# Kernel optimization log

Measured on AMD Instinct MI355X. Metric: run time of the kernel, lower is better.

## Reference

```python
import math
import jax, jax.numpy as jnp
import numpy as np

NUM_HEADS = 12
ALPHA, BETA, GAMMA = 1.9, 3.8, 15.2  # get_rpe_config(ratio=1.9)
SKIP = 1


def _rp_bucket(side):
    """iRPE euclidean contextual bucket table for a side x side grid + 1 cls token."""
    beta_int = int(BETA)
    coords = np.stack(np.meshgrid(np.arange(side), np.arange(side), indexing='ij'), -1).reshape(-1, 2)
    diff = coords[:, None, :] - coords[None, :, :]
    dis = np.round(np.sqrt((diff ** 2).sum(-1).astype(np.float64)))  # rounded euclidean distance
    far = np.clip(np.round(ALPHA + np.log(np.maximum(dis, 1e-9) / ALPHA) / math.log(GAMMA / ALPHA) * (BETA - ALPHA)), None, BETA)
    idx = np.where(dis <= ALPHA, dis, far).astype(np.int32) + beta_int
    num_buckets = 2 * beta_int + 1  # 7
    L = side * side
    full = np.full((L + SKIP, L + SKIP), num_buckets, dtype=np.int32)  # extra bucket for cls
    full[SKIP:, SKIP:] = idx
    return full, num_buckets + 1  # table [P,P], total buckets = 8


def setup_inputs() -> dict:
    key = jax.random.key(0)
    ks = jax.random.split(key, 8)
    B, P, n_mod, C = 64, 197, 2, 768
    N = 1 + (P - 1) * n_mod  # 393
    hd = C // NUM_HEADS
    rp_bucket, n_buckets = _rp_bucket(int(math.sqrt(P - SKIP)))
    s = 0.02
    return {
        'x': jax.random.normal(ks[0], (B, N, C), jnp.float32),
        'q_learned': jax.random.normal(ks[1], (1, 1, C), jnp.float32) * s,
        'pos_embed': jax.random.normal(ks[2], (1, P, C), jnp.float32) * s,
        'wk': jax.random.normal(ks[3], (C, C), jnp.float32) * s,
        'wv': jax.random.normal(ks[4], (C, C), jnp.float32) * s,
        'rpe_w': jax.random.normal(ks[5], (hd, n_buckets), jnp.float32) * s,  # shared_head ctx lookup table
        'proj_w': jax.random.normal(ks[6], (C, C), jnp.float32) * s,
        'proj_b': jnp.zeros((C,), jnp.float32),
        'rp_bucket': jnp.asarray(rp_bucket),  # [P, P] int32
    }


def reference(x, q_learned, pos_embed, wk, wv, rpe_w, proj_w, proj_b, rp_bucket):
    B, N, C = x.shape
    H = NUM_HEADS
    hd = C // H
    P = rp_bucket.shape[0]
    n_mod = (N - 1) // (P - 1)
    scale = hd ** -0.5

    q_ = jnp.broadcast_to(q_learned + pos_embed, (B, P, C))
    q = q_.reshape(B, P, H, hd).transpose(0, 2, 1, 3)                    # bhpd
    k = (x @ wk.T).reshape(B, N, H, hd).transpose(0, 2, 1, 3)            # bhnd
    v = (x @ wv.T).reshape(B, N, H, hd).transpose(0, 2, 1, 3)            # bhnd

    attn = jnp.einsum('bhpd,bhnd->bhpn', q, k) * scale                   # [B,H,P,N]

    # contextual RPE on keys: lookup = q @ table, gathered by rp_bucket[i, j]
    lookup = jnp.einsum('bhpd,du->bhpu', q, rpe_w)                        # [B,H,P,n_buckets]
    bias = lookup[:, :, jnp.arange(P)[:, None], rp_bucket]                # [B,H,P,P]
    bias = jnp.concatenate([bias[..., :1], jnp.tile(bias[..., 1:], (1, 1, 1, n_mod))], axis=-1)
    attn = jax.nn.softmax(attn + bias, axis=-1)

    out = jnp.einsum('bhpn,bhnd->bhpd', attn, v).transpose(0, 2, 1, 3).reshape(B, P, C)
    return out @ proj_w.T + proj_b
```

## Files before the change

### kernel.cpp

```cpp
#include <hip/hip_runtime.h>

typedef unsigned short u16;
typedef short bf16x8 __attribute__((ext_vector_type(8)));
typedef float f32x4 __attribute__((ext_vector_type(4)));
typedef const __attribute__((address_space(1))) void* gptr_t;
typedef __attribute__((address_space(3))) void* lptr_t;

#define B_   64
#define N_   393
#define C_   768
#define H_   12
#define HD_  64
#define P_   197
#define BIAS_N 416
#define PPAD 208
#define VTP  448
#define M_KV (B_ * N_)
#define M_PR (B_ * P_)
#define SCALE_L2E 0.180336879f
#define PPITCH 70

__device__ __forceinline__ u16 f2bf(float f) {
    unsigned u = __float_as_uint(f);
    return (u16)((u + 0x7FFFu + ((u >> 16) & 1u)) >> 16);
}
__device__ __forceinline__ unsigned cvt_pk_bf16(float lo, float hi) {
    unsigned r;
    asm("v_cvt_pk_bf16_f32 %0, %1, %2" : "=v"(r) : "v"(lo), "v"(hi));
    return r;
}
__device__ __forceinline__ float exp2_fast(float x) {
    float r;
    asm("v_exp_f32 %0, %1" : "=v"(r) : "v"(x));
    return r;
}

__global__ __launch_bounds__(256) void conv_prep1(
    const float* __restrict__ x, const float* __restrict__ wk,
    const float* __restrict__ wv, const float* __restrict__ pw,
    const float* __restrict__ q_learned, const float* __restrict__ pos_embed,
    const float* __restrict__ rpe_w,
    u16* __restrict__ xh, u16* __restrict__ wkvh, u16* __restrict__ pwh,
    u16* __restrict__ qh, float* __restrict__ lk)
{
    __shared__ float q_s[C_];
    const int bx = blockIdx.x, t = threadIdx.x;
    if (bx < 20592) {
        const int XN4 = 19316736 / 4;
        const int WN4 = 589824 / 4;
        int i = bx * 256 + t;
        const float* src; u16* dst; int off;
        if (i < XN4) { src = x; dst = xh; off = i; }
        else {
            int j = i - XN4;
            int sec = j / WN4;
            off = j - sec * WN4;
            src = sec == 0 ? wk : (sec == 1 ? wv : pw);
            dst = sec == 0 ? wkvh : (sec == 1 ? wkvh + 589824 : pwh);
        }
        float4 v = ((const float4*)src)[off];
        u16 o[4] = {f2bf(v.x), f2bf(v.y), f2bf(v.z), f2bf(v.w)};
        *(uint2*)(dst + off * 4) = *(uint2*)o;
    } else {
        const int p = bx - 20592;
        for (int c = t; c < C_; c += 256) {
            float v = q_learned[c] + pos_embed[p * C_ + c];
            q_s[c] = v;
            qh[p * C_ + c] = f2bf(v);
        }
        __syncthreads();
        if (t < H_ * 8) {
            int h = t >> 3, u = t & 7;
            float s = 0.f;
            #pragma unroll 8
            for (int d = 0; d < HD_; ++d)
                s = fmaf(q_s[h * HD_ + d], rpe_w[d * 8 + u], s);
            lk[(h * P_ + p) * 8 + u] = s;
        }
    }
}

__global__ __launch_bounds__(512) void gemm_kv512(
    const u16* __restrict__ A, const u16* __restrict__ Bw, u16* __restrict__ Cb)
{
    __shared__ __align__(16) u16 As[128 * 64];
    __shared__ __align__(16) u16 Bs[128 * 64];

    const int gx = gridDim.x;
    const int nwg = gx * gridDim.y;
    const int orig = blockIdx.y * gx + blockIdx.x;
    const int xcd = orig & 7, rank = orig >> 3;
    const int q = nwg >> 3, r = nwg & 7;
    const int wgid = (xcd < r ? xcd * (q + 1) : r * (q + 1) + (xcd - r) * q) + rank;
    const int n0 = (wgid % gx) * 128;
    const int m0 = (wgid / gx) * 128;

    const int t = threadIdx.x;
    const int wid = t >> 6, l = t & 63;
    const int wr = wid >> 2, wc = wid & 3;
    const int l15 = l & 15, lg = l >> 4;
    const int Mc = M_KV - 1;

    int srow[2], sslot[2];
    #pragma unroll
    for (int i = 0; i < 2; ++i) {
        int c = t + 512 * i;
        srow[i] = c >> 3; sslot[i] = c & 7;
    }

    f32x4 acc[4][2];
    #pragma unroll
    for (int i = 0; i < 4; ++i)
        #pragma unroll
        for (int j = 0; j < 2; ++j) acc[i][j] = (f32x4){0.f, 0.f, 0.f, 0.f};

    for (int ks = 0; ks < 12; ++ks) {
        const int k0 = ks * 64;
        if (ks) __syncthreads();
        #pragma unroll
        for (int i = 0; i < 2; ++i) {
            const int c = t + 512 * i;
            int arow = m0 + srow[i]; if (arow > Mc) arow = Mc;
            const u16* ga = A  + (size_t)arow * 768 + k0 + sslot[i] * 8;
            const u16* gb = Bw + (size_t)(n0 + srow[i]) * 768 + k0 + sslot[i] * 8;
            __builtin_amdgcn_global_load_lds((gptr_t)(const void*)ga,
                                             (lptr_t)(void*)(As + c * 8), 16, 0, 0);
            __builtin_amdgcn_global_load_lds((gptr_t)(const void*)gb,
                                             (lptr_t)(void*)(Bs + c * 8), 16, 0, 0);
        }
        __syncthreads();
        #pragma unroll
        for (int kk = 0; kk < 2; ++kk) {
            bf16x8 af[4], bfr[2];
            #pragma unroll
            for (int mf = 0; mf < 4; ++mf)
                af[mf] = *(const bf16x8*)(As + (wr * 64 + mf * 16 + l15) * 64 + (kk * 4 + lg) * 8);
            #pragma unroll
            for (int nf = 0; nf < 2; ++nf)
                bfr[nf] = *(const bf16x8*)(Bs + (wc * 32 + nf * 16 + l15) * 64 + (kk * 4 + lg) * 8);
            #pragma unroll
            for (int mf = 0; mf < 4; ++mf)
                #pragma unroll
                for (int nf = 0; nf < 2; ++nf)
                    acc[mf][nf] = __builtin_amdgcn_mfma_f32_16x16x32_bf16(
                        af[mf], bfr[nf], acc[mf][nf], 0, 0, 0);
        }
    }

    #pragma unroll
    for (int mf = 0; mf < 4; ++mf)
        #pragma unroll
        for (int nf = 0; nf < 2; ++nf) {
            int col = n0 + wc * 32 + nf * 16 + l15;
            #pragma unroll
            for (int rr = 0; rr < 4; ++rr) {
                int m = m0 + wr * 64 + mf * 16 + lg * 4 + rr;
                if (m < M_KV) Cb[(size_t)m * 1536 + col] = f2bf(acc[mf][nf][rr]);
            }
        }
}

__global__ __launch_bounds__(256) void gemm_proj(
    const u16* __restrict__ A, const u16* __restrict__ Bw,
    float* __restrict__ Cf, const float* __restrict__ bias)
{
    __shared__ __align__(16) u16 As[128 * 64];
    __shared__ __align__(16) u16 Bs[128 * 64];

    const int gx = gridDim.x;
    const int nwg = gx * gridDim.y;
    const int orig = blockIdx.y * gx + blockIdx.x;
    const int xcd = orig & 7, rank = orig >> 3;
    const int q = nwg >> 3, r = nwg & 7;
    const int wgid = (xcd < r ? xcd * (q + 1) : r * (q + 1) + (xcd - r) * q) + rank;
    const int n0 = (wgid % gx) * 128;
    const int m0 = (wgid / gx) * 128;

    const int t = threadIdx.x;
    const int w = t >> 6, l = t & 63;
    const int wr = w >> 1, wc = w & 1;
    const int l15 = l & 15, lg = l >> 4;
    const int lrow = l >> 3, lslot = l & 7;
    const int Mc = M_PR - 1;

    f32x4 acc[4][4];
    #pragma unroll
    for (int i = 0; i < 4; ++i)
        #pragma unroll
        for (int j = 0; j < 4; ++j) acc[i][j] = (f32x4){0.f, 0.f, 0.f, 0.f};

    for (int ks = 0; ks < 12; ++ks) {
        const int k0 = ks * 64;
        if (ks) __syncthreads();
        #pragma unroll
        for (int i = 0; i < 4; ++i) {
            const int rbase = w * 32 + i * 8;
            int arow = m0 + rbase + lrow; if (arow > Mc) arow = Mc;
            const int brow = n0 + rbase + lrow;
            const u16* ga = A  + (size_t)arow * 768 + k0 + lslot * 8;
            const u16* gb = Bw + (size_t)brow * 768 + k0 + lslot * 8;
            __builtin_amdgcn_global_load_lds((gptr_t)(const void*)ga,
                                             (lptr_t)(void*)(As + rbase * 64), 16, 0, 0);
            __builtin_amdgcn_global_load_lds((gptr_t)(const void*)gb,
                                             (lptr_t)(void*)(Bs + rbase * 64), 16, 0, 0);
        }
        __syncthreads();
        #pragma unroll
        for (int kk = 0; kk < 2; ++kk) {
            bf16x8 af[4], bfr[4];
            #pragma unroll
            for (int mf = 0; mf < 4; ++mf) {
                af[mf]  = *(const bf16x8*)(As + (wr * 64 + mf * 16 + l15) * 64 + (kk * 4 + lg) * 8);
                bfr[mf] = *(const bf16x8*)(Bs + (wc * 64 + mf * 16 + l15) * 64 + (kk * 4 + lg) * 8);
            }
            #pragma unroll
            for (int mf = 0; mf < 4; ++mf)
                #pragma unroll
                for (int nf = 0; nf < 4; ++nf)
                    acc[mf][nf] = __builtin_amdgcn_mfma_f32_16x16x32_bf16(
                        af[mf], bfr[nf], acc[mf][nf], 0, 0, 0);
        }
    }

    #pragma unroll
    for (int mf = 0; mf < 4; ++mf)
        #pragma unroll
        for (int nf = 0; nf < 4; ++nf) {
            int col = n0 + wc * 64 + nf * 16 + l15;
            float bb = bias[col];
            #pragma unroll
            for (int rr = 0; rr < 4; ++rr) {
                int m = m0 + wr * 64 + mf * 16 + lg * 4 + rr;
                if (m < M_PR) Cf[(size_t)m * 768 + col] = acc[mf][nf][rr] + bb;
            }
        }
}

__global__ __launch_bounds__(256) void vtrans_prep2(
    const u16* __restrict__ KV, u16* __restrict__ Vt,
    const float* __restrict__ lk, const int* __restrict__ rp_bucket,
    float* __restrict__ biasT2)
{
    __shared__ __align__(16) u16 vts[64][68];
    const int bx = blockIdx.x, t = threadIdx.x;
    if (bx < B_ * H_) {
        const int b = bx / H_, h = bx % H_;
        const u16* src = KV + (size_t)b * N_ * 1536 + 768 + h * HD_;
        u16* dst = Vt + (size_t)bx * HD_ * VTP;
        for (int jt = 0; jt < 7; ++jt) {
            const int j0 = jt * 64;
            if (jt) __syncthreads();
            #pragma unroll
            for (int ps = 0; ps < 2; ++ps) {
                int jr = ps * 32 + (t >> 3);
                int dd = (t & 7) * 8;
                int j = j0 + jr;
                bf16x8 v = (bf16x8){0, 0, 0, 0, 0, 0, 0, 0};
                if (j < N_) v = *(const bf16x8*)(src + (size_t)j * 1536 + dd);
                *(bf16x8*)(&vts[jr][dd]) = v;
            }
            __syncthreads();
            #pragma unroll
            for (int ps = 0; ps < 2; ++ps) {
                int idx = t + 256 * ps;
                int d = idx >> 3, ch = idx & 7;
                u16 v[8];
                #pragma unroll
                for (int k = 0; k < 8; ++k) v[k] = vts[ch * 8 + k][d];
                *(bf16x8*)(dst + (size_t)d * VTP + j0 + ch * 8) = *(bf16x8*)v;
            }
        }
    } else {
        const int i = bx - B_ * H_;
        const int h = i / PPAD, p = i % PPAD;
        for (int j = t; j < BIAS_N; j += 256) {
            float v = 0.f;
            if (p < P_ && j < N_) {
                int jm;
                if (j == 0) jm = 0;
                else { jm = j - 1; if (jm >= 196) jm -= 196; jm += 1; }
                int bucket = rp_bucket[p * P_ + jm];
                v = lk[(h * P_ + p) * 8 + bucket] * 1.44269504f;
            }
            biasT2[((size_t)h * PPAD + p) * BIAS_N + j] = v;
        }
    }
}

__global__ __launch_bounds__(256, 3) void attn_flash(
    const u16* __restrict__ qh, const u16* __restrict__ KV,
    const u16* __restrict__ Vt, const float* __restrict__ biasT2,
    u16* __restrict__ Obuf)
{
    __shared__ __align__(16) u16 kk[2][64 * 64];
    __shared__ __align__(16) u16 vv[2][64 * 64];
    __shared__ __align__(16) u16 pp[2][64 * PPITCH];

    const int id = blockIdx.x;
    const int work = (id & 7) * 384 + (id >> 3);
    const int ptile = work & 3;
    const int rest = work >> 2;
    const int h = rest % 12;
    const int b = rest / 12;
    const int p0 = ptile * 64;

    const int t = threadIdx.x, w = t >> 6, l = t & 63;
    const int l15 = l & 15, lg = l >> 4;
    const int p0w = p0 + w * 16;
    const int rowp = w * 16 + l15;

    int srow[2], sslot[2], swoff[2];
    #pragma unroll
    for (int i = 0; i < 2; ++i) {
        int c = t + 256 * i;
        srow[i] = c >> 3; sslot[i] = c & 7;
        swoff[i] = srow[i] * 64 + ((sslot[i] ^ (srow[i] & 7)) << 3);
    }

    int prow = p0w + l15; if (prow > P_ - 1) prow = P_ - 1;
    const u16* qp = qh + (size_t)prow * C_ + h * HD_ + lg * 8;
    bf16x8 qf0 = *(const bf16x8*)(qp);
    bf16x8 qf1 = *(const bf16x8*)(qp + 32);

    const u16* Kbase = KV + (size_t)b * (N_ * 1536) + h * HD_;
    const u16* Vbase = Vt + (size_t)(b * H_ + h) * (HD_ * VTP);
    const int pcl = (p0 + rowp) > (PPAD - 1) ? (PPAD - 1) : (p0 + rowp);
    const float* bias_row = biasT2 + ((size_t)h * PPAD + pcl) * BIAS_N;

    bf16x8 raK[2], raV[2];
    #pragma unroll
    for (int i = 0; i < 2; ++i)
        raK[i] = *(const bf16x8*)(Kbase + (size_t)srow[i] * 1536 + sslot[i] * 8);
    #pragma unroll
    for (int i = 0; i < 2; ++i) *(bf16x8*)(&kk[0][swoff[i]]) = raK[i];
    #pragma unroll
    for (int i = 0; i < 2; ++i) {
        int rn = 64 + srow[i]; if (rn > N_ - 1) rn = N_ - 1;
        raK[i] = *(const bf16x8*)(Kbase + (size_t)rn * 1536 + sslot[i] * 8);
    }
    #pragma unroll
    for (int i = 0; i < 2; ++i)
        raV[i] = *(const bf16x8*)(Vbase + (size_t)srow[i] * VTP + sslot[i] * 8);
    __syncthreads();

    float s_acc = 0.f;
    f32x4 o[4];
    #pragma unroll
    for (int i = 0; i < 4; ++i) o[i] = (f32x4){0.f, 0.f, 0.f, 0.f};

    #pragma unroll
    for (int nt = 0; nt < 7; ++nt) {
        const int cur = nt & 1, nxt = cur ^ 1;
        const u16* kcur = kk[cur];
        const int submax = (nt == 6) ? 1 : 4;

        f32x4 accs[4];
        #pragma unroll
        for (int i = 0; i < 4; ++i) accs[i] = (f32x4){0.f, 0.f, 0.f, 0.f};
        __builtin_amdgcn_s_setprio(1);
        #pragma unroll
        for (int kc = 0; kc < 2; ++kc)
            #pragma unroll
            for (int sub = 0; sub < 4; ++sub) {
                if (sub >= submax) continue;
                int row = sub * 16 + l15;
                bf16x8 kb = *(const bf16x8*)(kcur + row * 64 + (((kc * 4 + lg) ^ (row & 7)) << 3));
                accs[sub] = __builtin_amdgcn_mfma_f32_16x16x32_bf16(
                    kb, kc ? qf1 : qf0, accs[sub], 0, 0, 0);
            }
        __builtin_amdgcn_s_setprio(0);

        #pragma unroll
        for (int i = 0; i < 2; ++i) *(bf16x8*)(&vv[cur][swoff[i]]) = raV[i];
        if (nt < 6) {
            #pragma unroll
            for (int i = 0; i < 2; ++i) *(bf16x8*)(&kk[nxt][swoff[i]]) = raK[i];
        }
        if (nt < 5) {
            #pragma unroll
            for (int i = 0; i < 2; ++i) {
                int rn = (nt + 2) * 64 + srow[i]; if (rn > N_ - 1) rn = N_ - 1;
                raK[i] = *(const bf16x8*)(Kbase + (size_t)rn * 1536 + sslot[i] * 8);
            }
        }
        if (nt < 6) {
            #pragma unroll
            for (int i = 0; i < 2; ++i)
                raV[i] = *(const bf16x8*)(Vbase + (size_t)srow[i] * VTP + (nt + 1) * 64 + sslot[i] * 8);
        }

        #pragma unroll
        for (int sub = 0; sub < 4; ++sub) {
            if (sub >= submax) continue;
            int jb = nt * 64 + sub * 16 + lg * 4;
            float4 b4 = *(const float4*)(bias_row + jb);
            float bb[4] = {b4.x, b4.y, b4.z, b4.w};
            float e[4];
            #pragma unroll
            for (int rr = 0; rr < 4; ++rr) {
                float ev = exp2_fast(fmaf(accs[sub][rr], SCALE_L2E, bb[rr]));
                e[rr] = (jb + rr < N_) ? ev : 0.f;
                s_acc += e[rr];
            }
            unsigned pk01 = cvt_pk_bf16(e[0], e[1]);
            unsigned pk23 = cvt_pk_bf16(e[2], e[3]);
            *(unsigned*)(&pp[cur][rowp * PPITCH + sub * 16 + lg * 4]) = pk01;
            *(unsigned*)(&pp[cur][rowp * PPITCH + sub * 16 + lg * 4 + 2]) = pk23;
        }
        if (nt == 6) {
            *(unsigned*)(&pp[cur][rowp * PPITCH + 16 + lg * 4]) = 0;
            *(unsigned*)(&pp[cur][rowp * PPITCH + 16 + lg * 4 + 2]) = 0;
        }
        __syncthreads();

        const int kcmax = (nt == 6) ? 1 : 2;
        __builtin_amdgcn_s_setprio(1);
        #pragma unroll
        for (int kc = 0; kc < 2; ++kc) {
            if (kc >= kcmax) continue;
            bf16x8 pa = *(const bf16x8*)(&pp[cur][rowp * PPITCH + kc * 32 + lg * 8]);
            #pragma unroll
            for (int dsub = 0; dsub < 4; ++dsub) {
                int row = dsub * 16 + l15;
                bf16x8 vb = *(const bf16x8*)(&vv[cur][row * 64 + (((kc * 4 + lg) ^ (row & 7)) << 3)]);
                o[dsub] = __builtin_amdgcn_mfma_f32_16x16x32_bf16(vb, pa, o[dsub], 0, 0, 0);
            }
        }
        __builtin_amdgcn_s_setprio(0);
    }

    s_acc += __shfl_xor(s_acc, 16);
    s_acc += __shfl_xor(s_acc, 32);
    float rinv = 1.0f / s_acc;

    int p = p0 + rowp;
    if (p < P_) {
        #pragma unroll
        for (int dsub = 0; dsub < 4; ++dsub) {
            u16 v4[4];
            #pragma unroll
            for (int rr = 0; rr < 4; ++rr) v4[rr] = f2bf(o[dsub][rr] * rinv);
            *(uint2*)(Obuf + ((size_t)b * P_ + p) * C_ + h * HD_ + dsub * 16 + lg * 4) =
                *(uint2*)v4;
        }
    }
}

extern "C" void kernel_launch(void* const* d_in, const int* in_sizes, int n_in,
                              void* d_out, int out_size, void* d_ws, size_t ws_size,
                              hipStream_t stream)
{
    const float* x         = (const float*)d_in[0];
    const float* q_learned = (const float*)d_in[1];
    const float* pos_embed = (const float*)d_in[2];
    const float* wk        = (const float*)d_in[3];
    const float* wv        = (const float*)d_in[4];
    const float* rpe_w     = (const float*)d_in[5];
    const float* proj_w    = (const float*)d_in[6];
    const float* proj_b    = (const float*)d_in[7];
    const int*   rp_bucket = (const int*)d_in[8];
    float* out = (float*)d_out;

    char* ws = (char*)d_ws;
    u16*   xh    = (u16*)(ws);
    u16*   wkvh  = (u16*)(ws + 38633472);
    u16*   pwh   = (u16*)(ws + 40992768);
    u16*   qh    = (u16*)(ws + 42172416);
    float* lk    = (float*)(ws + 42475008);
    float* biasT2= (float*)(ws + 42550784);
    u16*   KV    = (u16*)(ws + 46704128);
    u16*   Vt    = (u16*)(ws + 123971072);
    u16*   Obuf  = (u16*)(ws + 168011264);

    conv_prep1<<<20789, 256, 0, stream>>>(x, wk, wv, proj_w,
                                          q_learned, pos_embed, rpe_w,
                                          xh, wkvh, pwh, qh, lk);

    dim3 gkv(1536 / 128, (M_KV + 127) / 128);
    gemm_kv512<<<gkv, 512, 0, stream>>>(xh, wkvh, KV);

    vtrans_prep2<<<3264, 256, 0, stream>>>(KV, Vt, lk, rp_bucket, biasT2);

    attn_flash<<<3072, 256, 0, stream>>>(qh, KV, Vt, biasT2, Obuf);

    dim3 gpr(768 / 128, (M_PR + 127) / 128);
    gemm_proj<<<gpr, 256, 0, stream>>>(Obuf, pwh, out, proj_b);
}
```

Before: 226.8 us.

## Fuse fp32-to-bf16 conversion of x into the KV GEMM A-tile load

The separate pass that converted x to bf16 in the prep kernel is removed. The KV GEMM now reads fp32 x directly, converts it in registers with v_cvt_pk_bf16, and writes it to LDS, which eliminates a full write and re-read of the ~38MB bf16 copy of x. The GEMM also moves from 512 to 256 threads with a 4x4 MFMA tile per wave. That raises register pressure, and because x tiles are re-read once per N tile (12 times) in fp32, A-side global traffic doubles.

```diff
diff --git a/kernel.cpp b/kernel.cpp
--- a/kernel.cpp
+++ b/kernel.cpp
@@ -36,33 +36,25 @@
 }
 
 __global__ __launch_bounds__(256) void conv_prep1(
-    const float* __restrict__ x, const float* __restrict__ wk,
-    const float* __restrict__ wv, const float* __restrict__ pw,
+    const float* __restrict__ wk, const float* __restrict__ wv,
+    const float* __restrict__ pw,
     const float* __restrict__ q_learned, const float* __restrict__ pos_embed,
     const float* __restrict__ rpe_w,
-    u16* __restrict__ xh, u16* __restrict__ wkvh, u16* __restrict__ pwh,
+    u16* __restrict__ wkvh, u16* __restrict__ pwh,
     u16* __restrict__ qh, float* __restrict__ lk)
 {
     __shared__ float q_s[C_];
     const int bx = blockIdx.x, t = threadIdx.x;
-    if (bx < 20592) {
-        const int XN4 = 19316736 / 4;
-        const int WN4 = 589824 / 4;
-        int i = bx * 256 + t;
-        const float* src; u16* dst; int off;
-        if (i < XN4) { src = x; dst = xh; off = i; }
-        else {
-            int j = i - XN4;
-            int sec = j / WN4;
-            off = j - sec * WN4;
-            src = sec == 0 ? wk : (sec == 1 ? wv : pw);
-            dst = sec == 0 ? wkvh : (sec == 1 ? wkvh + 589824 : pwh);
-        }
-        float4 v = ((const float4*)src)[off];
+    if (bx < 1728) {
+        int sec = bx / 576;
+        int i = (bx - sec * 576) * 256 + t;
+        const float* src = sec == 0 ? wk : (sec == 1 ? wv : pw);
+        u16* dst = sec == 0 ? wkvh : (sec == 1 ? wkvh + 589824 : pwh);
+        float4 v = ((const float4*)src)[i];
         u16 o[4] = {f2bf(v.x), f2bf(v.y), f2bf(v.z), f2bf(v.w)};
-        *(uint2*)(dst + off * 4) = *(uint2*)o;
+        *(uint2*)(dst + i * 4) = *(uint2*)o;
     } else {
-        const int p = bx - 20592;
+        const int p = bx - 1728;
         for (int c = t; c < C_; c += 256) {
             float v = q_learned[c] + pos_embed[p * C_ + c];
             q_s[c] = v;
@@ -80,8 +72,8 @@
     }
 }
 
-__global__ __launch_bounds__(512) void gemm_kv512(
-    const u16* __restrict__ A, const u16* __restrict__ Bw, u16* __restrict__ Cb)
+__global__ __launch_bounds__(256) void gemm_kv_fx(
+    const float* __restrict__ X, const u16* __restrict__ Bw, u16* __restrict__ Cb)
 {
     __shared__ __align__(16) u16 As[128 * 64];
     __shared__ __align__(16) u16 Bs[128 * 64];
@@ -96,52 +88,64 @@
     const int m0 = (wgid / gx) * 128;
 
     const int t = threadIdx.x;
-    const int wid = t >> 6, l = t & 63;
-    const int wr = wid >> 2, wc = wid & 3;
+    const int w = t >> 6, l = t & 63;
+    const int wr = w >> 1, wc = w & 1;
     const int l15 = l & 15, lg = l >> 4;
+    const int lrow = l >> 3, lslot = l & 7;
     const int Mc = M_KV - 1;
 
-    int srow[2], sslot[2];
-    #pragma unroll
-    for (int i = 0; i < 2; ++i) {
-        int c = t + 512 * i;
-        srow[i] = c >> 3; sslot[i] = c & 7;
-    }
-
-    f32x4 acc[4][2];
+    const float* gxp[4];
+    #pragma unroll
+    for (int i = 0; i < 4; ++i) {
+        int c = t + 256 * i;
+        int arow = m0 + (c >> 3); if (arow > Mc) arow = Mc;
+        gxp[i] = X + (size_t)arow * 768 + (c & 7) * 8;
+    }
+
+    f32x4 acc[4][4];
     #pragma unroll
     for (int i = 0; i < 4; ++i)
         #pragma unroll
-        for (int j = 0; j < 2; ++j) acc[i][j] = (f32x4){0.f, 0.f, 0.f, 0.f};
+        for (int j = 0; j < 4; ++j) acc[i][j] = (f32x4){0.f, 0.f, 0.f, 0.f};
 
     for (int ks = 0; ks < 12; ++ks) {
         const int k0 = ks * 64;
         if (ks) __syncthreads();
-        #pragma unroll
-        for (int i = 0; i < 2; ++i) {
-            const int c = t + 512 * i;
-            int arow = m0 + srow[i]; if (arow > Mc) arow = Mc;
-            const u16* ga = A  + (size_t)arow * 768 + k0 + sslot[i] * 8;
-            const u16* gb = Bw + (size_t)(n0 + srow[i]) * 768 + k0 + sslot[i] * 8;
-            __builtin_amdgcn_global_load_lds((gptr_t)(const void*)ga,
-                                             (lptr_t)(void*)(As + c * 8), 16, 0, 0);
+        float4 a0[4], a1[4];
+        #pragma unroll
+        for (int i = 0; i < 4; ++i) {
+            a0[i] = *(const float4*)(gxp[i] + k0);
+            a1[i] = *(const float4*)(gxp[i] + k0 + 4);
+        }
+        #pragma unroll
+        for (int i = 0; i < 4; ++i) {
+            const int rbase = w * 32 + i * 8;
+            const u16* gb = Bw + (size_t)(n0 + rbase + lrow) * 768 + k0 + lslot * 8;
             __builtin_amdgcn_global_load_lds((gptr_t)(const void*)gb,
-                                             (lptr_t)(void*)(Bs + c * 8), 16, 0, 0);
+                                             (lptr_t)(void*)(Bs + rbase * 64), 16, 0, 0);
+        }
+        #pragma unroll
+        for (int i = 0; i < 4; ++i) {
+            unsigned pk[4];
+            pk[0] = cvt_pk_bf16(a0[i].x, a0[i].y);
+            pk[1] = cvt_pk_bf16(a0[i].z, a0[i].w);
+            pk[2] = cvt_pk_bf16(a1[i].x, a1[i].y);
+            pk[3] = cvt_pk_bf16(a1[i].z, a1[i].w);
+            *(bf16x8*)(As + (t + 256 * i) * 8) = *(bf16x8*)pk;
         }
         __syncthreads();
         #pragma unroll
         for (int kk = 0; kk < 2; ++kk) {
-            bf16x8 af[4], bfr[2];
-            #pragma unroll
-            for (int mf = 0; mf < 4; ++mf)
-                af[mf] = *(const bf16x8*)(As + (wr * 64 + mf * 16 + l15) * 64 + (kk * 4 + lg) * 8);
-            #pragma unroll
-            for (int nf = 0; nf < 2; ++nf)
-                bfr[nf] = *(const bf16x8*)(Bs + (wc * 32 + nf * 16 + l15) * 64 + (kk * 4 + lg) * 8);
+            bf16x8 af[4], bfr[4];
+            #pragma unroll
+            for (int mf = 0; mf < 4; ++mf) {
+                af[mf]  = *(const bf16x8*)(As + (wr * 64 + mf * 16 + l15) * 64 + (kk * 4 + lg) * 8);
+                bfr[mf] = *(const bf16x8*)(Bs + (wc * 64 + mf * 16 + l15) * 64 + (kk * 4 + lg) * 8);
+            }
             #pragma unroll
             for (int mf = 0; mf < 4; ++mf)
                 #pragma unroll
-                for (int nf = 0; nf < 2; ++nf)
+                for (int nf = 0; nf < 4; ++nf)
                     acc[mf][nf] = __builtin_amdgcn_mfma_f32_16x16x32_bf16(
                         af[mf], bfr[nf], acc[mf][nf], 0, 0, 0);
         }
@@ -150,8 +154,8 @@
     #pragma unroll
     for (int mf = 0; mf < 4; ++mf)
         #pragma unroll
-        for (int nf = 0; nf < 2; ++nf) {
-            int col = n0 + wc * 32 + nf * 16 + l15;
+        for (int nf = 0; nf < 4; ++nf) {
+            int col = n0 + wc * 64 + nf * 16 + l15;
             #pragma unroll
             for (int rr = 0; rr < 4; ++rr) {
                 int m = m0 + wr * 64 + mf * 16 + lg * 4 + rr;
@@ -462,7 +466,6 @@
     float* out = (float*)d_out;
 
     char* ws = (char*)d_ws;
-    u16*   xh    = (u16*)(ws);
     u16*   wkvh  = (u16*)(ws + 38633472);
     u16*   pwh   = (u16*)(ws + 40992768);
     u16*   qh    = (u16*)(ws + 42172416);
@@ -472,12 +475,12 @@
     u16*   Vt    = (u16*)(ws + 123971072);
     u16*   Obuf  = (u16*)(ws + 168011264);
 
-    conv_prep1<<<20789, 256, 0, stream>>>(x, wk, wv, proj_w,
-                                          q_learned, pos_embed, rpe_w,
-                                          xh, wkvh, pwh, qh, lk);
+    conv_prep1<<<1925, 256, 0, stream>>>(wk, wv, proj_w,
+                                         q_learned, pos_embed, rpe_w,
+                                         wkvh, pwh, qh, lk);
 
     dim3 gkv(1536 / 128, (M_KV + 127) / 128);
-    gemm_kv512<<<gkv, 512, 0, stream>>>(xh, wkvh, KV);
+    gemm_kv_fx<<<gkv, 256, 0, stream>>>(x, wkvh, KV);
 
     vtrans_prep2<<<3264, 256, 0, stream>>>(KV, Vt, lk, rp_bucket, biasT2);
 
```

New measurement: 217.2 us. 4.2% less time.
